# Performance work log

Hardware: AMD Instinct MI355X
Metric: run time of the kernel (lower is better)

Reference implementation:

```python
import math
import jax, jax.numpy as jnp
import numpy as np

B, N_PER, FEAT, EMB, HEADS, E = 64, 512, 128, 128, 3, 131072
NEG = -1e9


def _gat(x, src, dst, emask, W, a_src, a_dst, bias):
    # PyG GATConv (concat heads, add_self_loops=True, negative_slope=0.2, eval mode -> no dropout)
    n = x.shape[0]
    H, C = a_src.shape
    h = (x @ W).reshape(n, H, C)                      # [n,H,C]
    e_src = (h * a_src[None]).sum(-1)                 # [n,H]
    e_dst = (h * a_dst[None]).sum(-1)                 # [n,H]
    loop = jnp.arange(n)
    s = jnp.concatenate([src, loop])
    d = jnp.concatenate([dst, loop])
    m = jnp.concatenate([emask, jnp.ones((n,), dtype=bool)])
    logit = jax.nn.leaky_relu(e_src[s] + e_dst[d], negative_slope=0.2)  # [E+n,H]
    logit = jnp.where(m[:, None], logit, NEG)
    mx = jax.ops.segment_max(logit, d, num_segments=n)
    ex = jnp.exp(logit - mx[d]) * m[:, None].astype(logit.dtype)
    den = jax.ops.segment_sum(ex, d, num_segments=n)
    alpha = ex / (den[d] + 1e-16)                     # edge-softmax over incoming edges
    out = jax.ops.segment_sum(alpha[:, :, None] * h[s], d, num_segments=n)
    return out.reshape(n, H * C) + bias


def _topk_pool(x, src, dst, emask, ratio, w):
    # PyG TopKPooling: score = tanh(x.w/||w||), keep ceil(ratio*n) per graph, gate kept x by score
    n = x.shape[0]
    per = n // B
    score = jnp.tanh((x @ w) / jnp.linalg.norm(w))    # [n]
    k = int(math.ceil(ratio * per))
    _, idx = jax.lax.top_k(score.reshape(B, per), k)  # [B,k]
    perm = (idx + (jnp.arange(B) * per)[:, None]).reshape(-1)
    xn = x[perm] * score[perm][:, None]
    newid = jnp.full((n,), -1, dtype=jnp.int32).at[perm].set(jnp.arange(B * k, dtype=jnp.int32))
    ns, nd = newid[src], newid[dst]
    valid = emask & (ns >= 0) & (nd >= 0)
    src = jnp.where(valid, ns, 0)
    dst = jnp.where(valid, nd, 0)
    batch = jnp.repeat(jnp.arange(B, dtype=jnp.int32), k)
    return xn, src, dst, valid, batch


def _gpool(x, batch):
    # cat([global_max_pool, global_mean_pool])
    mx = jax.ops.segment_max(x, batch, num_segments=B)
    sm = jax.ops.segment_sum(x, batch, num_segments=B)
    cnt = jax.ops.segment_sum(jnp.ones((x.shape[0], 1), x.dtype), batch, num_segments=B)
    return jnp.concatenate([mx, sm / cnt], axis=1)


def _forward(x, edge_attr, edge_index, batch_index, params):
    (W1, as1, ad1, b1, Wh1, bh1, pw1,
     W2, as2, ad2, b2, Wh2, bh2, pw2,
     W3, as3, ad3, b3, Wh3, bh3, pw3,
     Wl1, bl1, Wl2, bl2) = params
    src, dst = edge_index[0], edge_index[1]
    emask = jnp.ones((src.shape[0],), dtype=bool)

    h = _gat(x, src, dst, emask, W1, as1, ad1, b1)
    h = jax.nn.relu(h @ Wh1 + bh1)
    h, src, dst, emask, batch = _topk_pool(h, src, dst, emask, 0.8, pw1)
    x1 = _gpool(h, batch)

    h = _gat(h, src, dst, emask, W2, as2, ad2, b2)
    h = jax.nn.relu(h @ Wh2 + bh2)
    h, src, dst, emask, batch = _topk_pool(h, src, dst, emask, 0.5, pw2)
    x2 = _gpool(h, batch)

    h = _gat(h, src, dst, emask, W3, as3, ad3, b3)
    h = jax.nn.relu(h @ Wh3 + bh3)
    h, src, dst, emask, batch = _topk_pool(h, src, dst, emask, 0.2, pw3)
    x3 = _gpool(h, batch)

    z = x1 + x2 + x3
    z = jax.nn.relu(z @ Wl1 + bl1)
    # F.dropout p=0.8 skipped (eval mode)
    return z @ Wl2 + bl2


def setup_inputs() -> dict:
    key = jax.random.key(0)
    ks = jax.random.split(key, 32)
    e_per = E // B
    e = jax.random.randint(ks[0], (2, B, e_per), 0, N_PER) + (jnp.arange(B) * N_PER)[None, :, None]
    edge_index = e.reshape(2, E).astype(jnp.int32)
    inp = {
        'x': jax.random.normal(ks[1], (B * N_PER, FEAT), dtype=jnp.float32),
        'edge_attr': jnp.zeros((E, 1), dtype=jnp.float32),
        'edge_index': edge_index,
        'batch_index': jnp.repeat(jnp.arange(B, dtype=jnp.int32), N_PER),
    }
    def rn(k, shape, s=0.1):
        return jax.random.normal(k, shape, dtype=jnp.float32) * s
    names = ['W1','as1','ad1','b1','Wh1','bh1','pw1',
             'W2','as2','ad2','b2','Wh2','bh2','pw2',
             'W3','as3','ad3','b3','Wh3','bh3','pw3',
             'Wl1','bl1','Wl2','bl2']
    shapes = [(FEAT, HEADS*EMB), (HEADS, EMB), (HEADS, EMB), (HEADS*EMB,), (HEADS*EMB, EMB), (EMB,), (EMB,),
              (EMB, HEADS*EMB), (HEADS, EMB), (HEADS, EMB), (HEADS*EMB,), (HEADS*EMB, EMB), (EMB,), (EMB,),
              (EMB, HEADS*EMB), (HEADS, EMB), (HEADS, EMB), (HEADS*EMB,), (HEADS*EMB, EMB), (EMB,), (EMB,),
              (2*EMB, 512), (512,), (512, 256), (256,)]
    for i, (nm, sh) in enumerate(zip(names, shapes)):
        inp[nm] = rn(ks[2 + i], sh)
    return inp


def reference(x, edge_attr, edge_index, batch_index,
              W1, as1, ad1, b1, Wh1, bh1, pw1,
              W2, as2, ad2, b2, Wh2, bh2, pw2,
              W3, as3, ad3, b3, Wh3, bh3, pw3,
              Wl1, bl1, Wl2, bl2):
    params = (W1, as1, ad1, b1, Wh1, bh1, pw1,
              W2, as2, ad2, b2, Wh2, bh2, pw2,
              W3, as3, ad3, b3, Wh3, bh3, pw3,
              Wl1, bl1, Wl2, bl2)
    return _forward(x, edge_attr, edge_index, batch_index, params)
```

## Files before the change

kernel.cpp:

```cpp
#include <hip/hip_runtime.h>
#include <cfloat>

static __device__ __forceinline__ float lrelu(float v) { return v >= 0.f ? v : 0.2f * v; }

typedef __attribute__((ext_vector_type(8))) short bf16x8;
typedef __attribute__((ext_vector_type(8))) unsigned short ushort8;
typedef __attribute__((ext_vector_type(4))) float f32x4;

__device__ __forceinline__ unsigned short f2bf(float x) {
    unsigned u = __float_as_uint(x);
    u += 0x7FFF + ((u >> 16) & 1);
    return (unsigned short)(u >> 16);
}
__device__ __forceinline__ float bf2f(unsigned short h) {
    return __uint_as_float(((unsigned)h) << 16);
}

struct SegT { const float* s; unsigned short* dh; unsigned short* dl; int rows, cols, tr; };
struct Segs { SegT seg[7]; int cum[8]; };

__global__ __launch_bounds__(256) void split_k(Segs S, int total)
{
    int idx = blockIdx.x * 256 + threadIdx.x;
    if (idx >= total) return;
    int si = 0;
    while (idx >= S.cum[si + 1]) si++;
    int o = idx - S.cum[si];
    SegT g = S.seg[si];
    float v = g.s[o];
    unsigned short h = f2bf(v);
    unsigned short l = f2bf(v - bf2f(h));
    int di = o;
    if (g.tr) { int r = o / g.cols, c = o - r * g.cols; di = c * g.rows + r; }
    g.dh[di] = h;
    g.dl[di] = l;
}

__global__ __launch_bounds__(192) void rn3_k(const float* __restrict__ pw0,
                                             const float* __restrict__ pw1,
                                             const float* __restrict__ pw2,
                                             float* __restrict__ rn)
{
    int l = threadIdx.x >> 6, lane = threadIdx.x & 63;
    const float* pw = (l == 0) ? pw0 : ((l == 1) ? pw1 : pw2);
    float v0 = pw[lane], v1 = pw[lane + 64];
    float p = v0 * v0 + v1 * v1;
#pragma unroll
    for (int o = 32; o > 0; o >>= 1) p += __shfl_down(p, o);
    if (lane == 0) rn[l] = 1.f / sqrtf(p);
}

__global__ __launch_bounds__(256) void gemm_bf2_k(const unsigned short* __restrict__ AH,
                                                  const unsigned short* __restrict__ AL,
                                                  const unsigned short* __restrict__ BTH,
                                                  const unsigned short* __restrict__ BTL,
                                                  const float* __restrict__ bias,
                                                  float* __restrict__ C,
                                                  int M, int K, int N, int relu,
                                                  const float* __restrict__ pwv,
                                                  const float* __restrict__ rnormp,
                                                  float* __restrict__ scv,
                                                  const float* __restrict__ asv,
                                                  const float* __restrict__ adv,
                                                  float* __restrict__ esv,
                                                  float* __restrict__ edv)
{
    __shared__ unsigned short sAH[64 * 64], sAL[64 * 64];
    __shared__ unsigned short sBH[128 * 64], sBL[128 * 64];
    __shared__ float sred[4][64];
    const int tid  = threadIdx.x;
    const int lane = tid & 63;
    const int wave = tid >> 6;
    const int wr = (wave >> 1) * 32;
    const int wc = (wave & 1) * 64;
    const int row0 = blockIdx.x * 64, col0 = blockIdx.y * 128;

    f32x4 acc[2][4];
#pragma unroll
    for (int i = 0; i < 2; i++)
#pragma unroll
        for (int j = 0; j < 4; j++) acc[i][j] = (f32x4){0.f, 0.f, 0.f, 0.f};

    const int a_r  = tid >> 2;
    const int a_cp = (tid & 3) * 2;
    const unsigned short* ApH = AH + (size_t)(row0 + a_r) * K + a_cp * 8;
    const unsigned short* ApL = AL + (size_t)(row0 + a_r) * K + a_cp * 8;
    const int a_sw = a_r & 7;
    const int a_s0 = a_r * 64 + (((a_cp + 0) ^ a_sw) << 3);
    const int a_s1 = a_r * 64 + (((a_cp + 1) ^ a_sw) << 3);

    const int b_c  = tid >> 1;
    const int b_cp = (tid & 1) * 4;
    const unsigned short* BpH = BTH + (size_t)(col0 + b_c) * K + b_cp * 8;
    const unsigned short* BpL = BTL + (size_t)(col0 + b_c) * K + b_cp * 8;
    const int b_sw = b_c & 7;
    int b_s[4];
#pragma unroll
    for (int i = 0; i < 4; i++) b_s[i] = b_c * 64 + (((b_cp + i) ^ b_sw) << 3);

    const int l15 = lane & 15;
    const int kc  = lane >> 4;

    for (int k0 = 0; k0 < K; k0 += 64) {
        ushort8 vah0 = *reinterpret_cast<const ushort8*>(ApH + k0);
        ushort8 vah1 = *reinterpret_cast<const ushort8*>(ApH + k0 + 8);
        ushort8 val0 = *reinterpret_cast<const ushort8*>(ApL + k0);
        ushort8 val1 = *reinterpret_cast<const ushort8*>(ApL + k0 + 8);
        ushort8 vbh[4], vbl[4];
#pragma unroll
        for (int i = 0; i < 4; i++) {
            vbh[i] = *reinterpret_cast<const ushort8*>(BpH + k0 + i * 8);
            vbl[i] = *reinterpret_cast<const ushort8*>(BpL + k0 + i * 8);
        }

        __syncthreads();

        *reinterpret_cast<ushort8*>(&sAH[a_s0]) = vah0;
        *reinterpret_cast<ushort8*>(&sAH[a_s1]) = vah1;
        *reinterpret_cast<ushort8*>(&sAL[a_s0]) = val0;
        *reinterpret_cast<ushort8*>(&sAL[a_s1]) = val1;
#pragma unroll
        for (int i = 0; i < 4; i++) {
            *reinterpret_cast<ushort8*>(&sBH[b_s[i]]) = vbh[i];
            *reinterpret_cast<ushort8*>(&sBL[b_s[i]]) = vbl[i];
        }
        __syncthreads();

#pragma unroll
        for (int ks = 0; ks < 2; ks++) {
            const int ch = ks * 4 + kc;
            bf16x8 aH[2], aL[2], bH[4], bL[4];
#pragma unroll
            for (int fi = 0; fi < 2; fi++) {
                int r = wr + fi * 16 + l15;
                int sidx = r * 64 + ((ch ^ (r & 7)) << 3);
                aH[fi] = *reinterpret_cast<const bf16x8*>(&sAH[sidx]);
                aL[fi] = *reinterpret_cast<const bf16x8*>(&sAL[sidx]);
            }
#pragma unroll
            for (int fj = 0; fj < 4; fj++) {
                int c = wc + fj * 16 + l15;
                int sidx = c * 64 + ((ch ^ (c & 7)) << 3);
                bH[fj] = *reinterpret_cast<const bf16x8*>(&sBH[sidx]);
                bL[fj] = *reinterpret_cast<const bf16x8*>(&sBL[sidx]);
            }
#pragma unroll
            for (int fi = 0; fi < 2; fi++)
#pragma unroll
                for (int fj = 0; fj < 4; fj++) {
                    acc[fi][fj] = __builtin_amdgcn_mfma_f32_16x16x32_bf16(aH[fi], bH[fj], acc[fi][fj], 0, 0, 0);
                    acc[fi][fj] = __builtin_amdgcn_mfma_f32_16x16x32_bf16(aH[fi], bL[fj], acc[fi][fj], 0, 0, 0);
                    acc[fi][fj] = __builtin_amdgcn_mfma_f32_16x16x32_bf16(aL[fi], bH[fj], acc[fi][fj], 0, 0, 0);
                }
        }
    }

    float pwl[4], asl[4], adl[4];
    if (scv) {
#pragma unroll
        for (int fj = 0; fj < 4; fj++) pwl[fj] = pwv[wc + fj * 16 + l15];
    }
    const int hd = blockIdx.y;
    if (esv) {
#pragma unroll
        for (int fj = 0; fj < 4; fj++) {
            int cl = wc + fj * 16 + l15;
            asl[fj] = asv[hd * 128 + cl];
            adl[fj] = adv[hd * 128 + cl];
        }
    }
    float pd[2][4]  = {{0.f,0.f,0.f,0.f},{0.f,0.f,0.f,0.f}};
    float pds[2][4] = {{0.f,0.f,0.f,0.f},{0.f,0.f,0.f,0.f}};
    float pdd[2][4] = {{0.f,0.f,0.f,0.f},{0.f,0.f,0.f,0.f}};
#pragma unroll
    for (int fi = 0; fi < 2; fi++) {
        int rbase = row0 + wr + fi * 16 + (lane >> 4) * 4;
#pragma unroll
        for (int q = 0; q < 4; q++) {
            int r = rbase + q;
#pragma unroll
            for (int fj = 0; fj < 4; fj++) {
                int c = col0 + wc + fj * 16 + l15;
                float v = acc[fi][fj][q];
                if (bias) v += bias[c];
                if (relu) v = fmaxf(v, 0.f);
                C[(size_t)r * N + c] = v;
                if (scv) pd[fi][q] += v * pwl[fj];
                if (esv) { pds[fi][q] += v * asl[fj]; pdd[fi][q] += v * adl[fj]; }
            }
        }
    }
    if (scv) {
        float rn0 = rnormp[0];
#pragma unroll
        for (int fi = 0; fi < 2; fi++)
#pragma unroll
            for (int q = 0; q < 4; q++) {
                float s = pd[fi][q];
                s += __shfl_xor(s, 1);
                s += __shfl_xor(s, 2);
                s += __shfl_xor(s, 4);
                s += __shfl_xor(s, 8);
                if (l15 == 0) sred[wc >> 6][wr + fi * 16 + (lane >> 4) * 4 + q] = s;
            }
        __syncthreads();
        if (tid < 64)
            scv[row0 + tid] = tanhf((sred[0][tid] + sred[1][tid]) * rn0);
    }
    if (esv) {
#pragma unroll
        for (int fi = 0; fi < 2; fi++)
#pragma unroll
            for (int q = 0; q < 4; q++) {
                float s = pds[fi][q];
                s += __shfl_xor(s, 1);
                s += __shfl_xor(s, 2);
                s += __shfl_xor(s, 4);
                s += __shfl_xor(s, 8);
                float d = pdd[fi][q];
                d += __shfl_xor(d, 1);
                d += __shfl_xor(d, 2);
                d += __shfl_xor(d, 4);
                d += __shfl_xor(d, 8);
                if (l15 == 0) {
                    int rl = wr + fi * 16 + (lane >> 4) * 4 + q;
                    sred[wc >> 6][rl] = s;
                    sred[2 + (wc >> 6)][rl] = d;
                }
            }
        __syncthreads();
        if (tid < 64) {
            int r = row0 + tid;
            esv[(size_t)r * 3 + hd] = sred[0][tid] + sred[1][tid];
            edv[(size_t)r * 3 + hd] = sred[2][tid] + sred[3][tid];
        }
    }
}

__global__ __launch_bounds__(256) void gemm_small_k(const float* __restrict__ A,
                                                    const float* __restrict__ B,
                                                    const float* __restrict__ bias,
                                                    float* __restrict__ C,
                                                    int M, int K, int N, int relu)
{
    int idx = blockIdx.x * 256 + threadIdx.x;
    if (idx >= M * N) return;
    int r = idx / N, c = idx - r * N;
    const float* ap = A + (size_t)r * K;
    const float* bp = B + c;
    float s = 0.f;
#pragma unroll 8
    for (int k = 0; k < K; k++) s += ap[k] * bp[(size_t)k * N];
    if (bias) s += bias[c];
    if (relu) s = fmaxf(s, 0.f);
    C[idx] = s;
}

__global__ __launch_bounds__(256) void csr_k(const int* __restrict__ src,
                                             const int* __restrict__ dst,
                                             const int* __restrict__ valid,
                                             const float* __restrict__ es,
                                             const float* __restrict__ ed,
                                             int* __restrict__ csr,
                                             int* __restrict__ beg,
                                             int* __restrict__ end,
                                             float* __restrict__ wmx,
                                             float* __restrict__ winv,
                                             float* __restrict__ wself,
                                             int per)
{
    __shared__ int sdeg[512];
    __shared__ int soff[512];
    __shared__ float ses[1536];
    __shared__ float sed[1536];
    const int g = blockIdx.x;
    const int t = threadIdx.x;
    const int bn = g * per;
    const int be = g * 2048;
    for (int i = t; i < 512; i += 256) sdeg[i] = 0;
    for (int i = t; i < per * 3; i += 256) {
        ses[i] = es[(size_t)bn * 3 + i];
        sed[i] = ed[(size_t)bn * 3 + i];
    }
    __syncthreads();
#pragma unroll
    for (int j = 0; j < 8; j++) {
        int e = be + j * 256 + t;
        if (!valid || valid[e]) atomicAdd(&sdeg[dst[e] - bn], 1);
    }
    __syncthreads();
    const int i0 = t, i1 = t + 256;
    soff[i0] = sdeg[i0]; soff[i1] = sdeg[i1];
    __syncthreads();
    for (int d = 1; d < 512; d <<= 1) {
        int a0 = (i0 >= d) ? soff[i0 - d] : 0;
        int a1 = (i1 >= d) ? soff[i1 - d] : 0;
        __syncthreads();
        soff[i0] += a0; soff[i1] += a1;
        __syncthreads();
    }
    int excl0 = 0, excl1 = 0;
    if (i0 < per) { int dg = sdeg[i0]; excl0 = soff[i0] - dg; beg[bn + i0] = be + excl0; end[bn + i0] = be + excl0 + dg; }
    if (i1 < per) { int dg = sdeg[i1]; excl1 = soff[i1] - dg; beg[bn + i1] = be + excl1; end[bn + i1] = be + excl1 + dg; }
    __syncthreads();
    if (i0 < per) { soff[i0] = excl0; sdeg[i0] = excl0; }
    if (i1 < per) { soff[i1] = excl1; sdeg[i1] = excl1; }
    __syncthreads();
#pragma unroll
    for (int j = 0; j < 8; j++) {
        int e = be + j * 256 + t;
        if (!valid || valid[e]) {
            int p = atomicAdd(&sdeg[dst[e] - bn], 1);
            csr[be + p] = e;
        }
    }
    __syncthreads();
    for (int i = t; i < per; i += 256) {
        float edv[3], m[3], den[3], selfl[3];
#pragma unroll
        for (int h = 0; h < 3; h++) {
            edv[h] = sed[i * 3 + h];
            selfl[h] = lrelu(ses[i * 3 + h] + edv[h]);
            m[h] = selfl[h];
            den[h] = 1.f;
        }
        const int pb = soff[i], pe = sdeg[i];
        for (int p = pb; p < pe; p++) {
            int e = csr[be + p];
            int sl = src[e] - bn;
#pragma unroll
            for (int h = 0; h < 3; h++) {
                float l = lrelu(ses[sl * 3 + h] + edv[h]);
                if (l <= m[h]) den[h] += __expf(l - m[h]);
                else { den[h] = den[h] * __expf(m[h] - l) + 1.f; m[h] = l; }
            }
        }
#pragma unroll
        for (int h = 0; h < 3; h++) {
            float inv = 1.f / (den[h] + 1e-16f);
            wmx[(size_t)(bn + i) * 3 + h] = m[h];
            winv[(size_t)(bn + i) * 3 + h] = inv;
            wself[(size_t)(bn + i) * 3 + h] = __expf(selfl[h] - m[h]) * inv;
        }
    }
}

__global__ __launch_bounds__(256) void agg2_k(const float* __restrict__ H,
                                              const float* __restrict__ es,
                                              const float* __restrict__ ed,
                                              const float* __restrict__ wmx,
                                              const float* __restrict__ winv,
                                              const float* __restrict__ wself,
                                              const int* __restrict__ beg,
                                              const int* __restrict__ end,
                                              const int* __restrict__ csr,
                                              const int* __restrict__ srcArr,
                                              const float* __restrict__ bias,
                                              unsigned short* __restrict__ outH,
                                              unsigned short* __restrict__ outL, int n)
{
    int nwg = gridDim.x;
    int bid = blockIdx.x;
    int swz = (bid & 7) * (nwg >> 3) + (bid >> 3);
    int wid = swz * 4 + (int)(threadIdx.x >> 6);
    int lane = threadIdx.x & 63;
    if (wid >= n) return;
    const int d = wid;
    float edv[3], mxv[3], ivv[3], wsf[3];
#pragma unroll
    for (int h = 0; h < 3; h++) {
        edv[h] = ed[(size_t)d * 3 + h];
        mxv[h] = wmx[(size_t)d * 3 + h];
        ivv[h] = winv[(size_t)d * 3 + h];
        wsf[h] = wself[(size_t)d * 3 + h];
    }
    float acc[6];
    const float* hp = H + (size_t)d * 384;
#pragma unroll
    for (int j = 0; j < 6; j++) acc[j] = wsf[j >> 1] * hp[lane + 64 * j];
    const int pb = beg[d], pe = end[d];
    int p = pb;
    for (; p + 2 <= pe; p += 2) {
        int e0 = csr[p], e1 = csr[p + 1];
        int s0 = srcArr[e0], s1 = srcArr[e1];
        float w0[3], w1[3];
#pragma unroll
        for (int h = 0; h < 3; h++) {
            float l0 = lrelu(es[(size_t)s0 * 3 + h] + edv[h]);
            float l1 = lrelu(es[(size_t)s1 * 3 + h] + edv[h]);
            w0[h] = __expf(l0 - mxv[h]) * ivv[h];
            w1[h] = __expf(l1 - mxv[h]) * ivv[h];
        }
        const float* sp0 = H + (size_t)s0 * 384;
        const float* sp1 = H + (size_t)s1 * 384;
#pragma unroll
        for (int j = 0; j < 6; j++)
            acc[j] += w0[j >> 1] * sp0[lane + 64 * j] + w1[j >> 1] * sp1[lane + 64 * j];
    }
    if (p < pe) {
        int eg = csr[p];
        int s = srcArr[eg];
        float w[3];
#pragma unroll
        for (int h = 0; h < 3; h++) {
            float l = lrelu(es[(size_t)s * 3 + h] + edv[h]);
            w[h] = __expf(l - mxv[h]) * ivv[h];
        }
        const float* sp = H + (size_t)s * 384;
#pragma unroll
        for (int j = 0; j < 6; j++)
            acc[j] += w[j >> 1] * sp[lane + 64 * j];
    }
#pragma unroll
    for (int j = 0; j < 6; j++) {
        float v = acc[j] + bias[lane + 64 * j];
        unsigned short h = f2bf(v);
        outH[(size_t)d * 384 + lane + 64 * j] = h;
        outL[(size_t)d * 384 + lane + 64 * j] = f2bf(v - bf2f(h));
    }
}

__global__ __launch_bounds__(512) void select_k(const float* __restrict__ sc,
                                                const int* __restrict__ s_old,
                                                const int* __restrict__ d_old,
                                                const int* __restrict__ v_old,
                                                int per, int k,
                                                int* __restrict__ perm, float* __restrict__ ps,
                                                int* __restrict__ s_new,
                                                int* __restrict__ d_new,
                                                int* __restrict__ v_new)
{
    __shared__ float ss[512];
    __shared__ int sid[512];
    __shared__ int snew[512];
    const int b = blockIdx.x;
    const int t = threadIdx.x;
    const int bn = b * per;

    ss[t] = (t < per) ? sc[bn + t] : -FLT_MAX;
    sid[t] = (t < per) ? t : 512 + t;
    __syncthreads();
    for (int kk = 2; kk <= 512; kk <<= 1)
        for (int j = kk >> 1; j > 0; j >>= 1) {
            int ixj = t ^ j;
            if (ixj > t) {
                float a = ss[t], bq = ss[ixj];
                int ia = sid[t], ib = sid[ixj];
                bool aBefore = (a > bq) || (a == bq && ia < ib);
                bool up = ((t & kk) == 0);
                if (up ? !aBefore : aBefore) { ss[t] = bq; ss[ixj] = a; sid[t] = ib; sid[ixj] = ia; }
            }
            __syncthreads();
        }
    if (sid[t] < per) snew[sid[t]] = (t < k) ? (b * k + t) : -1;
    if (t < k) {
        perm[b * k + t] = bn + sid[t];
        ps[b * k + t] = ss[t];
    }
    __syncthreads();

    if (s_new) {
        const int be = b * 2048;
#pragma unroll
        for (int j = 0; j < 4; j++) {
            int e = be + j * 512 + t;
            int v = v_old ? v_old[e] : 1;
            int ns = -1, nd = -1;
            if (v) { ns = snew[s_old[e] - bn]; nd = snew[d_old[e] - bn]; }
            int ok = (v && ns >= 0 && nd >= 0) ? 1 : 0;
            s_new[e] = ok ? ns : 0;
            d_new[e] = ok ? nd : 0;
            v_new[e] = ok;
        }
    }
}

__global__ __launch_bounds__(256) void gate_k(const float* __restrict__ H,
                                              const int* __restrict__ perm,
                                              const float* __restrict__ ps,
                                              float* __restrict__ X,
                                              unsigned short* __restrict__ XH,
                                              unsigned short* __restrict__ XL, int nNew)
{
    int wid = (int)((blockIdx.x * 256 + threadIdx.x) >> 6);
    int lane = threadIdx.x & 63;
    if (wid >= nNew) return;
    int o = perm[wid];
    float g = ps[wid];
    float v0 = H[(size_t)o * 128 + lane] * g;
    float v1 = H[(size_t)o * 128 + 64 + lane] * g;
    X[(size_t)wid * 128 + lane] = v0;
    X[(size_t)wid * 128 + 64 + lane] = v1;
    unsigned short h0 = f2bf(v0), h1 = f2bf(v1);
    XH[(size_t)wid * 128 + lane] = h0;
    XH[(size_t)wid * 128 + 64 + lane] = h1;
    XL[(size_t)wid * 128 + lane] = f2bf(v0 - bf2f(h0));
    XL[(size_t)wid * 128 + 64 + lane] = f2bf(v1 - bf2f(h1));
}

__global__ __launch_bounds__(1024) void gpool3_k(const float* __restrict__ X1,
                                                 const float* __restrict__ X2,
                                                 const float* __restrict__ X3,
                                                 int k1, int k2, int k3,
                                                 float* __restrict__ z)
{
    __shared__ float smx[8][128];
    __shared__ float ssm[8][128];
    const int b = blockIdx.x;
    const int col = threadIdx.x & 127;
    const int rg = threadIdx.x >> 7;
    const float* Xs[3] = {X1, X2, X3};
    const int ks[3] = {k1, k2, k3};
    float accm = 0.f, accs = 0.f;
#pragma unroll
    for (int L = 0; L < 3; L++) {
        const int k = ks[L];
        const float* xp = Xs[L] + (size_t)b * k * 128 + col;
        float mx = -FLT_MAX, sm = 0.f;
        int r = rg;
#pragma unroll 4
        for (; r + 32 <= k; r += 32) {
            float v0 = xp[(size_t)(r + 0)  * 128];
            float v1 = xp[(size_t)(r + 8)  * 128];
            float v2 = xp[(size_t)(r + 16) * 128];
            float v3 = xp[(size_t)(r + 24) * 128];
            mx = fmaxf(fmaxf(fmaxf(mx, v0), fmaxf(v1, v2)), v3);
            sm += v0 + v1 + v2 + v3;
        }
        for (; r < k; r += 8) {
            float v = xp[(size_t)r * 128];
            mx = fmaxf(mx, v);
            sm += v;
        }
        smx[rg][col] = mx;
        ssm[rg][col] = sm;
        __syncthreads();
        if (rg == 0) {
#pragma unroll
            for (int i = 1; i < 8; i++) { mx = fmaxf(mx, smx[i][col]); sm += ssm[i][col]; }
            accm += mx;
            accs += sm / (float)k;
        }
        __syncthreads();
    }
    if (rg == 0) {
        z[b * 256 + col] = accm;
        z[b * 256 + 128 + col] = accs;
    }
}

extern "C" void kernel_launch(void* const* d_in, const int* in_sizes, int n_in,
                              void* d_out, int out_size, void* d_ws, size_t ws_size,
                              hipStream_t stream)
{
    (void)in_sizes; (void)n_in; (void)out_size; (void)ws_size;

    const float* x   = (const float*)d_in[0];
    const int*   ei  = (const int*)d_in[2];
    const float* W1  = (const float*)d_in[4];
    const float* as1 = (const float*)d_in[5];
    const float* ad1 = (const float*)d_in[6];
    const float* b1  = (const float*)d_in[7];
    const float* Wh1 = (const float*)d_in[8];
    const float* bh1 = (const float*)d_in[9];
    const float* pw1 = (const float*)d_in[10];
    const float* W2  = (const float*)d_in[11];
    const float* as2 = (const float*)d_in[12];
    const float* ad2 = (const float*)d_in[13];
    const float* b2  = (const float*)d_in[14];
    const float* Wh2 = (const float*)d_in[15];
    const float* bh2 = (const float*)d_in[16];
    const float* pw2 = (const float*)d_in[17];
    const float* W3  = (const float*)d_in[18];
    const float* as3 = (const float*)d_in[19];
    const float* ad3 = (const float*)d_in[20];
    const float* b3  = (const float*)d_in[21];
    const float* Wh3 = (const float*)d_in[22];
    const float* bh3 = (const float*)d_in[23];
    const float* pw3 = (const float*)d_in[24];
    const float* Wl1 = (const float*)d_in[25];
    const float* bl1 = (const float*)d_in[26];
    const float* Wl2 = (const float*)d_in[27];
    const float* bl2 = (const float*)d_in[28];
    float* out = (float*)d_out;

    const int E = 131072;
    const int n1 = 32768, per1 = 512, k1 = 410;
    const int n2 = 64 * k1, per2 = k1, k2 = 205;
    const int n3 = 64 * k2, per3 = k2, k3 = 41;
    const int n4 = 64 * k3;

    char* wsb = (char*)d_ws;
    size_t off = 0;
    auto alloc = [&](size_t bytes) -> void* {
        void* p = wsb + off;
        off += (bytes + 255) & ~(size_t)255;
        return p;
    };
    float* A    = (float*)alloc((size_t)n1 * 384 * 4);
    unsigned short* BfH = (unsigned short*)alloc((size_t)n1 * 384 * 2);
    unsigned short* BfL = (unsigned short*)alloc((size_t)n1 * 384 * 2);
    unsigned short* X0H = (unsigned short*)alloc((size_t)n1 * 128 * 2);
    unsigned short* X0L = (unsigned short*)alloc((size_t)n1 * 128 * 2);
    unsigned short* XaH = (unsigned short*)alloc((size_t)n2 * 128 * 2);
    unsigned short* XaL = (unsigned short*)alloc((size_t)n2 * 128 * 2);
    unsigned short* WT[6], *WTl[6];
    for (int i = 0; i < 6; i++) {
        WT[i]  = (unsigned short*)alloc((size_t)49152 * 2);
        WTl[i] = (unsigned short*)alloc((size_t)49152 * 2);
    }
    float* ES   = (float*)alloc((size_t)n1 * 3 * 4);
    float* ED   = (float*)alloc((size_t)n1 * 3 * 4);
    float* SC   = (float*)alloc((size_t)n1 * 4);
    int*   CSR  = (int*)alloc((size_t)E * 4);
    int*   BEG  = (int*)alloc((size_t)n1 * 4);
    int*   END  = (int*)alloc((size_t)n1 * 4);
    int*   SRCA = (int*)alloc((size_t)E * 4);
    int*   DSTA = (int*)alloc((size_t)E * 4);
    int*   VALA = (int*)alloc((size_t)E * 4);
    int*   SRCB = (int*)alloc((size_t)E * 4);
    int*   DSTB = (int*)alloc((size_t)E * 4);
    int*   VALB = (int*)alloc((size_t)E * 4);
    float* X1   = (float*)alloc((size_t)n2 * 128 * 4);
    float* X2   = (float*)alloc((size_t)n3 * 128 * 4);
    float* X3   = (float*)alloc((size_t)n4 * 128 * 4);
    int*   PERM = (int*)alloc((size_t)n2 * 4);
    float* PSC  = (float*)alloc((size_t)n2 * 4);
    float* WMX  = (float*)alloc((size_t)n1 * 3 * 4);
    float* WINV = (float*)alloc((size_t)n1 * 3 * 4);
    float* WSELF= (float*)alloc((size_t)n1 * 3 * 4);
    float* RN   = (float*)alloc((size_t)4 * 4);
    float* Z    = (float*)alloc((size_t)64 * 256 * 4);
    float* ZH   = (float*)alloc((size_t)64 * 512 * 4);

    {
        Segs S;
        const float* srcs[7] = {x, W1, Wh1, W2, Wh2, W3, Wh3};
        unsigned short* dh[7] = {X0H, WT[0], WT[1], WT[2], WT[3], WT[4], WT[5]};
        unsigned short* dl[7] = {X0L, WTl[0], WTl[1], WTl[2], WTl[3], WTl[4], WTl[5]};
        int rows[7] = {n1, 128, 384, 128, 384, 128, 384};
        int cols[7] = {128, 384, 128, 384, 128, 384, 128};
        int trs[7]  = {0, 1, 1, 1, 1, 1, 1};
        int cum = 0;
        for (int i = 0; i < 7; i++) {
            S.seg[i] = SegT{srcs[i], dh[i], dl[i], rows[i], cols[i], trs[i]};
            S.cum[i] = cum;
            cum += rows[i] * cols[i];
        }
        S.cum[7] = cum;
        split_k<<<(cum + 255) / 256, 256, 0, stream>>>(S, cum);
        rn3_k<<<1, 192, 0, stream>>>(pw1, pw2, pw3, RN);
    }

    auto layer = [&](const unsigned short* xh, const unsigned short* xl,
                     int n, int per, int kk, int lidx,
                     const int* src, const int* dst, const int* val,
                     const unsigned short* wt, const unsigned short* wtl,
                     const float* as_, const float* ad_, const float* bb,
                     const unsigned short* wht, const unsigned short* whtl, const float* bh,
                     const float* pw,
                     float* Xn, unsigned short* XnH, unsigned short* XnL,
                     int* srcN, int* dstN, int* valN)
    {
        int nNew = 64 * kk;
        gemm_bf2_k<<<dim3(n / 64, 3), 256, 0, stream>>>(xh, xl, wt, wtl, nullptr, A, n, 128, 384, 0,
                                                        nullptr, nullptr, nullptr,
                                                        as_, ad_, ES, ED);
        csr_k<<<64, 256, 0, stream>>>(src, dst, val, ES, ED, CSR, BEG, END, WMX, WINV, WSELF, per);
        agg2_k<<<n / 4, 256, 0, stream>>>(A, ES, ED, WMX, WINV, WSELF, BEG, END, CSR, src, bb, BfH, BfL, n);
        gemm_bf2_k<<<dim3(n / 64, 1), 256, 0, stream>>>(BfH, BfL, wht, whtl, bh, A, n, 384, 128, 1,
                                                        pw, RN + lidx, SC,
                                                        nullptr, nullptr, nullptr, nullptr);
        select_k<<<64, 512, 0, stream>>>(SC, src, dst, val, per, kk, PERM, PSC, srcN, dstN, valN);
        gate_k<<<nNew / 4, 256, 0, stream>>>(A, PERM, PSC, Xn, XnH, XnL, nNew);
    };

    layer(X0H, X0L, n1, per1, k1, 0, ei,   ei + E, nullptr,
          WT[0], WTl[0], as1, ad1, b1, WT[1], WTl[1], bh1, pw1,
          X1, XaH, XaL, SRCA, DSTA, VALA);
    layer(XaH, XaL, n2, per2, k2, 1, SRCA, DSTA, VALA,
          WT[2], WTl[2], as2, ad2, b2, WT[3], WTl[3], bh2, pw2,
          X2, XaH, XaL, SRCB, DSTB, VALB);
    layer(XaH, XaL, n3, per3, k3, 2, SRCB, DSTB, VALB,
          WT[4], WTl[4], as3, ad3, b3, WT[5], WTl[5], bh3, pw3,
          X3, XaH, XaL, nullptr, nullptr, nullptr);

    gpool3_k<<<64, 1024, 0, stream>>>(X1, X2, X3, k1, k2, k3, Z);

    gemm_small_k<<<(64 * 512 + 255) / 256, 256, 0, stream>>>(Z,  Wl1, bl1, ZH,  64, 256, 512, 1);
    gemm_small_k<<<(64 * 256 + 255) / 256, 256, 0, stream>>>(ZH, Wl2, bl2, out, 64, 512, 256, 0);
}
```

Measured before the change: 349.9 us.

## Fuse rn3 into split, fuse pooling with MLP head, widen csr blocks

Folds the weight-norm kernel into the split kernel's last block, and merges global pooling with both MLP layers into one kernel, removing three launches. The fp32 copies of pooled features are dropped: gate writes only the bf16 hi/lo pairs, and pooling reconstructs values from them, saving global writes. csr_k now runs 512 threads per graph so each thread owns one node, which simplifies the scan. Risks: the MLP now runs on only 64 blocks with serial dot products, and the per-layer bf16 buffers are no longer shared.

```diff
diff --git a/kernel.cpp b/kernel.cpp
--- a/kernel.cpp
+++ b/kernel.cpp
@@ -19,8 +19,24 @@
 struct SegT { const float* s; unsigned short* dh; unsigned short* dl; int rows, cols, tr; };
 struct Segs { SegT seg[7]; int cum[8]; };
 
-__global__ __launch_bounds__(256) void split_k(Segs S, int total)
-{
+__global__ __launch_bounds__(256) void split_k(Segs S, int total,
+                                               const float* __restrict__ pw0,
+                                               const float* __restrict__ pw1,
+                                               const float* __restrict__ pw2,
+                                               float* __restrict__ rn)
+{
+    if (blockIdx.x == gridDim.x - 1) {
+        if (threadIdx.x < 192) {
+            int l = threadIdx.x >> 6, lane = threadIdx.x & 63;
+            const float* pw = (l == 0) ? pw0 : ((l == 1) ? pw1 : pw2);
+            float v0 = pw[lane], v1 = pw[lane + 64];
+            float p = v0 * v0 + v1 * v1;
+#pragma unroll
+            for (int o = 32; o > 0; o >>= 1) p += __shfl_down(p, o);
+            if (lane == 0) rn[l] = 1.f / sqrtf(p);
+        }
+        return;
+    }
     int idx = blockIdx.x * 256 + threadIdx.x;
     if (idx >= total) return;
     int si = 0;
@@ -34,20 +50,6 @@
     if (g.tr) { int r = o / g.cols, c = o - r * g.cols; di = c * g.rows + r; }
     g.dh[di] = h;
     g.dl[di] = l;
-}
-
-__global__ __launch_bounds__(192) void rn3_k(const float* __restrict__ pw0,
-                                             const float* __restrict__ pw1,
-                                             const float* __restrict__ pw2,
-                                             float* __restrict__ rn)
-{
-    int l = threadIdx.x >> 6, lane = threadIdx.x & 63;
-    const float* pw = (l == 0) ? pw0 : ((l == 1) ? pw1 : pw2);
-    float v0 = pw[lane], v1 = pw[lane + 64];
-    float p = v0 * v0 + v1 * v1;
-#pragma unroll
-    for (int o = 32; o > 0; o >>= 1) p += __shfl_down(p, o);
-    if (lane == 0) rn[l] = 1.f / sqrtf(p);
 }
 
 __global__ __launch_bounds__(256) void gemm_bf2_k(const unsigned short* __restrict__ AH,
@@ -237,26 +239,7 @@
     }
 }
 
-__global__ __launch_bounds__(256) void gemm_small_k(const float* __restrict__ A,
-                                                    const float* __restrict__ B,
-                                                    const float* __restrict__ bias,
-                                                    float* __restrict__ C,
-                                                    int M, int K, int N, int relu)
-{
-    int idx = blockIdx.x * 256 + threadIdx.x;
-    if (idx >= M * N) return;
-    int r = idx / N, c = idx - r * N;
-    const float* ap = A + (size_t)r * K;
-    const float* bp = B + c;
-    float s = 0.f;
-#pragma unroll 8
-    for (int k = 0; k < K; k++) s += ap[k] * bp[(size_t)k * N];
-    if (bias) s += bias[c];
-    if (relu) s = fmaxf(s, 0.f);
-    C[idx] = s;
-}
-
-__global__ __launch_bounds__(256) void csr_k(const int* __restrict__ src,
+__global__ __launch_bounds__(512) void csr_k(const int* __restrict__ src,
                                              const int* __restrict__ dst,
                                              const int* __restrict__ valid,
                                              const float* __restrict__ es,
@@ -277,54 +260,51 @@
     const int t = threadIdx.x;
     const int bn = g * per;
     const int be = g * 2048;
-    for (int i = t; i < 512; i += 256) sdeg[i] = 0;
-    for (int i = t; i < per * 3; i += 256) {
+    sdeg[t] = 0;
+    for (int i = t; i < per * 3; i += 512) {
         ses[i] = es[(size_t)bn * 3 + i];
         sed[i] = ed[(size_t)bn * 3 + i];
     }
     __syncthreads();
 #pragma unroll
-    for (int j = 0; j < 8; j++) {
-        int e = be + j * 256 + t;
+    for (int j = 0; j < 4; j++) {
+        int e = be + j * 512 + t;
         if (!valid || valid[e]) atomicAdd(&sdeg[dst[e] - bn], 1);
     }
     __syncthreads();
-    const int i0 = t, i1 = t + 256;
-    soff[i0] = sdeg[i0]; soff[i1] = sdeg[i1];
+    soff[t] = sdeg[t];
     __syncthreads();
     for (int d = 1; d < 512; d <<= 1) {
-        int a0 = (i0 >= d) ? soff[i0 - d] : 0;
-        int a1 = (i1 >= d) ? soff[i1 - d] : 0;
-        __syncthreads();
-        soff[i0] += a0; soff[i1] += a1;
-        __syncthreads();
-    }
-    int excl0 = 0, excl1 = 0;
-    if (i0 < per) { int dg = sdeg[i0]; excl0 = soff[i0] - dg; beg[bn + i0] = be + excl0; end[bn + i0] = be + excl0 + dg; }
-    if (i1 < per) { int dg = sdeg[i1]; excl1 = soff[i1] - dg; beg[bn + i1] = be + excl1; end[bn + i1] = be + excl1 + dg; }
-    __syncthreads();
-    if (i0 < per) { soff[i0] = excl0; sdeg[i0] = excl0; }
-    if (i1 < per) { soff[i1] = excl1; sdeg[i1] = excl1; }
-    __syncthreads();
-#pragma unroll
-    for (int j = 0; j < 8; j++) {
-        int e = be + j * 256 + t;
+        int v = (t >= d) ? soff[t - d] : 0;
+        __syncthreads();
+        soff[t] += v;
+        __syncthreads();
+    }
+    const int deg_t = sdeg[t];
+    const int excl = soff[t] - deg_t;
+    if (t < per) { beg[bn + t] = be + excl; end[bn + t] = be + excl + deg_t; }
+    __syncthreads();
+    sdeg[t] = excl;
+    __syncthreads();
+#pragma unroll
+    for (int j = 0; j < 4; j++) {
+        int e = be + j * 512 + t;
         if (!valid || valid[e]) {
             int p = atomicAdd(&sdeg[dst[e] - bn], 1);
             csr[be + p] = e;
         }
     }
     __syncthreads();
-    for (int i = t; i < per; i += 256) {
+    if (t < per) {
         float edv[3], m[3], den[3], selfl[3];
 #pragma unroll
         for (int h = 0; h < 3; h++) {
-            edv[h] = sed[i * 3 + h];
-            selfl[h] = lrelu(ses[i * 3 + h] + edv[h]);
+            edv[h] = sed[t * 3 + h];
+            selfl[h] = lrelu(ses[t * 3 + h] + edv[h]);
             m[h] = selfl[h];
             den[h] = 1.f;
         }
-        const int pb = soff[i], pe = sdeg[i];
+        const int pb = excl, pe = excl + deg_t;
         for (int p = pb; p < pe; p++) {
             int e = csr[be + p];
             int sl = src[e] - bn;
@@ -338,9 +318,9 @@
 #pragma unroll
         for (int h = 0; h < 3; h++) {
             float inv = 1.f / (den[h] + 1e-16f);
-            wmx[(size_t)(bn + i) * 3 + h] = m[h];
-            winv[(size_t)(bn + i) * 3 + h] = inv;
-            wself[(size_t)(bn + i) * 3 + h] = __expf(selfl[h] - m[h]) * inv;
+            wmx[(size_t)(bn + t) * 3 + h] = m[h];
+            winv[(size_t)(bn + t) * 3 + h] = inv;
+            wself[(size_t)(bn + t) * 3 + h] = __expf(selfl[h] - m[h]) * inv;
         }
     }
 }
@@ -478,7 +458,6 @@
 __global__ __launch_bounds__(256) void gate_k(const float* __restrict__ H,
                                               const int* __restrict__ perm,
                                               const float* __restrict__ ps,
-                                              float* __restrict__ X,
                                               unsigned short* __restrict__ XH,
                                               unsigned short* __restrict__ XL, int nNew)
 {
@@ -489,8 +468,6 @@
     float g = ps[wid];
     float v0 = H[(size_t)o * 128 + lane] * g;
     float v1 = H[(size_t)o * 128 + 64 + lane] * g;
-    X[(size_t)wid * 128 + lane] = v0;
-    X[(size_t)wid * 128 + 64 + lane] = v1;
     unsigned short h0 = f2bf(v0), h1 = f2bf(v1);
     XH[(size_t)wid * 128 + lane] = h0;
     XH[(size_t)wid * 128 + 64 + lane] = h1;
@@ -498,37 +475,49 @@
     XL[(size_t)wid * 128 + 64 + lane] = f2bf(v1 - bf2f(h1));
 }
 
-__global__ __launch_bounds__(1024) void gpool3_k(const float* __restrict__ X1,
-                                                 const float* __restrict__ X2,
-                                                 const float* __restrict__ X3,
-                                                 int k1, int k2, int k3,
-                                                 float* __restrict__ z)
+__global__ __launch_bounds__(1024) void gpoolmlp_k(const unsigned short* __restrict__ X1H,
+                                                   const unsigned short* __restrict__ X1L,
+                                                   const unsigned short* __restrict__ X2H,
+                                                   const unsigned short* __restrict__ X2L,
+                                                   const unsigned short* __restrict__ X3H,
+                                                   const unsigned short* __restrict__ X3L,
+                                                   int k1, int k2, int k3,
+                                                   const float* __restrict__ Wl1,
+                                                   const float* __restrict__ bl1,
+                                                   const float* __restrict__ Wl2,
+                                                   const float* __restrict__ bl2,
+                                                   float* __restrict__ out)
 {
     __shared__ float smx[8][128];
     __shared__ float ssm[8][128];
+    __shared__ float zrow[256];
+    __shared__ float hid[512];
     const int b = blockIdx.x;
-    const int col = threadIdx.x & 127;
-    const int rg = threadIdx.x >> 7;
-    const float* Xs[3] = {X1, X2, X3};
+    const int t = threadIdx.x;
+    const int col = t & 127;
+    const int rg = t >> 7;
+    const unsigned short* XsH[3] = {X1H, X2H, X3H};
+    const unsigned short* XsL[3] = {X1L, X2L, X3L};
     const int ks[3] = {k1, k2, k3};
     float accm = 0.f, accs = 0.f;
 #pragma unroll
     for (int L = 0; L < 3; L++) {
         const int k = ks[L];
-        const float* xp = Xs[L] + (size_t)b * k * 128 + col;
+        const unsigned short* xh = XsH[L] + (size_t)b * k * 128 + col;
+        const unsigned short* xl = XsL[L] + (size_t)b * k * 128 + col;
         float mx = -FLT_MAX, sm = 0.f;
         int r = rg;
 #pragma unroll 4
         for (; r + 32 <= k; r += 32) {
-            float v0 = xp[(size_t)(r + 0)  * 128];
-            float v1 = xp[(size_t)(r + 8)  * 128];
-            float v2 = xp[(size_t)(r + 16) * 128];
-            float v3 = xp[(size_t)(r + 24) * 128];
+            float v0 = bf2f(xh[(size_t)(r + 0)  * 128]) + bf2f(xl[(size_t)(r + 0)  * 128]);
+            float v1 = bf2f(xh[(size_t)(r + 8)  * 128]) + bf2f(xl[(size_t)(r + 8)  * 128]);
+            float v2 = bf2f(xh[(size_t)(r + 16) * 128]) + bf2f(xl[(size_t)(r + 16) * 128]);
+            float v3 = bf2f(xh[(size_t)(r + 24) * 128]) + bf2f(xl[(size_t)(r + 24) * 128]);
             mx = fmaxf(fmaxf(fmaxf(mx, v0), fmaxf(v1, v2)), v3);
             sm += v0 + v1 + v2 + v3;
         }
         for (; r < k; r += 8) {
-            float v = xp[(size_t)r * 128];
+            float v = bf2f(xh[(size_t)r * 128]) + bf2f(xl[(size_t)r * 128]);
             mx = fmaxf(mx, v);
             sm += v;
         }
@@ -544,8 +533,22 @@
         __syncthreads();
     }
     if (rg == 0) {
-        z[b * 256 + col] = accm;
-        z[b * 256 + 128 + col] = accs;
+        zrow[col] = accm;
+        zrow[128 + col] = accs;
+    }
+    __syncthreads();
+    if (t < 512) {
+        float s = bl1[t];
+#pragma unroll 4
+        for (int c = 0; c < 256; c++) s += zrow[c] * Wl1[(size_t)c * 512 + t];
+        hid[t] = fmaxf(s, 0.f);
+    }
+    __syncthreads();
+    if (t < 256) {
+        float s = bl2[t];
+#pragma unroll 4
+        for (int c = 0; c < 512; c++) s += hid[c] * Wl2[(size_t)c * 256 + t];
+        out[b * 256 + t] = s;
     }
 }
 
@@ -602,8 +605,12 @@
     unsigned short* BfL = (unsigned short*)alloc((size_t)n1 * 384 * 2);
     unsigned short* X0H = (unsigned short*)alloc((size_t)n1 * 128 * 2);
     unsigned short* X0L = (unsigned short*)alloc((size_t)n1 * 128 * 2);
-    unsigned short* XaH = (unsigned short*)alloc((size_t)n2 * 128 * 2);
-    unsigned short* XaL = (unsigned short*)alloc((size_t)n2 * 128 * 2);
+    unsigned short* X1H = (unsigned short*)alloc((size_t)n2 * 128 * 2);
+    unsigned short* X1L = (unsigned short*)alloc((size_t)n2 * 128 * 2);
+    unsigned short* X2H = (unsigned short*)alloc((size_t)n3 * 128 * 2);
+    unsigned short* X2L = (unsigned short*)alloc((size_t)n3 * 128 * 2);
+    unsigned short* X3H = (unsigned short*)alloc((size_t)n4 * 128 * 2);
+    unsigned short* X3L = (unsigned short*)alloc((size_t)n4 * 128 * 2);
     unsigned short* WT[6], *WTl[6];
     for (int i = 0; i < 6; i++) {
         WT[i]  = (unsigned short*)alloc((size_t)49152 * 2);
@@ -621,17 +628,12 @@
     int*   SRCB = (int*)alloc((size_t)E * 4);
     int*   DSTB = (int*)alloc((size_t)E * 4);
     int*   VALB = (int*)alloc((size_t)E * 4);
-    float* X1   = (float*)alloc((size_t)n2 * 128 * 4);
-    float* X2   = (float*)alloc((size_t)n3 * 128 * 4);
-    float* X3   = (float*)alloc((size_t)n4 * 128 * 4);
     int*   PERM = (int*)alloc((size_t)n2 * 4);
     float* PSC  = (float*)alloc((size_t)n2 * 4);
     float* WMX  = (float*)alloc((size_t)n1 * 3 * 4);
     float* WINV = (float*)alloc((size_t)n1 * 3 * 4);
     float* WSELF= (float*)alloc((size_t)n1 * 3 * 4);
     float* RN   = (float*)alloc((size_t)4 * 4);
-    float* Z    = (float*)alloc((size_t)64 * 256 * 4);
-    float* ZH   = (float*)alloc((size_t)64 * 512 * 4);
 
     {
         Segs S;
@@ -648,8 +650,7 @@
             cum += rows[i] * cols[i];
         }
         S.cum[7] = cum;
-        split_k<<<(cum + 255) / 256, 256, 0, stream>>>(S, cum);
-        rn3_k<<<1, 192, 0, stream>>>(pw1, pw2, pw3, RN);
+        split_k<<<(cum + 255) / 256 + 1, 256, 0, stream>>>(S, cum, pw1, pw2, pw3, RN);
     }
 
     auto layer = [&](const unsigned short* xh, const unsigned short* xl,
@@ -659,34 +660,32 @@
                      const float* as_, const float* ad_, const float* bb,
                      const unsigned short* wht, const unsigned short* whtl, const float* bh,
                      const float* pw,
-                     float* Xn, unsigned short* XnH, unsigned short* XnL,
+                     unsigned short* XnH, unsigned short* XnL,
                      int* srcN, int* dstN, int* valN)
     {
         int nNew = 64 * kk;
         gemm_bf2_k<<<dim3(n / 64, 3), 256, 0, stream>>>(xh, xl, wt, wtl, nullptr, A, n, 128, 384, 0,
                                                         nullptr, nullptr, nullptr,
                                                         as_, ad_, ES, ED);
-        csr_k<<<64, 256, 0, stream>>>(src, dst, val, ES, ED, CSR, BEG, END, WMX, WINV, WSELF, per);
+        csr_k<<<64, 512, 0, stream>>>(src, dst, val, ES, ED, CSR, BEG, END, WMX, WINV, WSELF, per);
         agg2_k<<<n / 4, 256, 0, stream>>>(A, ES, ED, WMX, WINV, WSELF, BEG, END, CSR, src, bb, BfH, BfL, n);
         gemm_bf2_k<<<dim3(n / 64, 1), 256, 0, stream>>>(BfH, BfL, wht, whtl, bh, A, n, 384, 128, 1,
                                                         pw, RN + lidx, SC,
                                                         nullptr, nullptr, nullptr, nullptr);
         select_k<<<64, 512, 0, stream>>>(SC, src, dst, val, per, kk, PERM, PSC, srcN, dstN, valN);
-        gate_k<<<nNew / 4, 256, 0, stream>>>(A, PERM, PSC, Xn, XnH, XnL, nNew);
+        gate_k<<<nNew / 4, 256, 0, stream>>>(A, PERM, PSC, XnH, XnL, nNew);
     };
 
     layer(X0H, X0L, n1, per1, k1, 0, ei,   ei + E, nullptr,
           WT[0], WTl[0], as1, ad1, b1, WT[1], WTl[1], bh1, pw1,
-          X1, XaH, XaL, SRCA, DSTA, VALA);
-    layer(XaH, XaL, n2, per2, k2, 1, SRCA, DSTA, VALA,
+          X1H, X1L, SRCA, DSTA, VALA);
+    layer(X1H, X1L, n2, per2, k2, 1, SRCA, DSTA, VALA,
           WT[2], WTl[2], as2, ad2, b2, WT[3], WTl[3], bh2, pw2,
-          X2, XaH, XaL, SRCB, DSTB, VALB);
-    layer(XaH, XaL, n3, per3, k3, 2, SRCB, DSTB, VALB,
+          X2H, X2L, SRCB, DSTB, VALB);
+    layer(X2H, X2L, n3, per3, k3, 2, SRCB, DSTB, VALB,
           WT[4], WTl[4], as3, ad3, b3, WT[5], WTl[5], bh3, pw3,
-          X3, XaH, XaL, nullptr, nullptr, nullptr);
-
-    gpool3_k<<<64, 1024, 0, stream>>>(X1, X2, X3, k1, k2, k3, Z);
-
-    gemm_small_k<<<(64 * 512 + 255) / 256, 256, 0, stream>>>(Z,  Wl1, bl1, ZH,  64, 256, 512, 1);
-    gemm_small_k<<<(64 * 256 + 255) / 256, 256, 0, stream>>>(ZH, Wl2, bl2, out, 64, 512, 256, 0);
-}
+          X3H, X3L, nullptr, nullptr, nullptr);
+
+    gpoolmlp_k<<<64, 1024, 0, stream>>>(X1H, X1L, X2H, X2L, X3H, X3L, k1, k2, k3,
+                                        Wl1, bl1, Wl2, bl2, out);
+}
```

After: 343.7 us. No clear change (-1.8%).
